# Performance work log

Measured on AMD Instinct MI355X. Metric: run time of the kernel, lower is better.

The kernel has to match this reference:

```python
import jax, jax.numpy as jnp
import numpy as np

NA, NT, E = 8000, 30000, 150000
H, C, HID = 4, 64, 64  # heads, per-head out_channels, hidden_dim
AF, TF = 32, 48


def _gat(x_src, x_dst, src, dst, W, a_src, a_dst, bias, n_dst):
    # PyG GATConv, concat=False, add_self_loops=False, eval (no dropout)
    h_src = (x_src @ W).reshape(-1, H, C)          # [Ns,H,C]
    h_dst = (x_dst @ W).reshape(-1, H, C)          # [Nd,H,C]
    al_s = jnp.sum(h_src * a_src, axis=-1)         # [Ns,H]
    al_d = jnp.sum(h_dst * a_dst, axis=-1)         # [Nd,H]
    e = jax.nn.leaky_relu(al_s[src] + al_d[dst], 0.2)  # [E,H]
    m = jax.ops.segment_max(e, dst, num_segments=n_dst)
    m = jnp.where(jnp.isfinite(m), m, 0.0)
    ex = jnp.exp(e - m[dst])
    den = jax.ops.segment_sum(ex, dst, num_segments=n_dst)
    alpha = ex / (den[dst] + 1e-16)                # per-dst softmax
    out = jax.ops.segment_sum(alpha[:, :, None] * h_src[src], dst, num_segments=n_dst)
    return jnp.mean(out, axis=1) + bias            # mean over heads + bias


def _bn(x, g, b):  # BatchNorm1d, training-mode batch stats, biased var
    mu = jnp.mean(x, axis=0)
    v = jnp.var(x, axis=0)
    return g * (x - mu) * jax.lax.rsqrt(v + 1e-5) + b


def _ln(x, g, b):
    mu = jnp.mean(x, axis=-1, keepdims=True)
    v = jnp.var(x, axis=-1, keepdims=True)
    return g * (x - mu) * jax.lax.rsqrt(v + 1e-5) + b


def setup_inputs() -> dict:
    key = jax.random.key(0)
    ks = jax.random.split(key, 40)
    n = lambda i, shp, s=0.05: jax.random.normal(ks[i], shp, jnp.float32) * s
    ri = lambda i, hi: jax.random.randint(ks[i], (E,), 0, hi, jnp.int32)
    inp = {
        'x_agent': jax.random.normal(ks[0], (NA, AF), jnp.float32),
        'x_track': jax.random.normal(ks[1], (NT, TF), jnp.float32),
        'ei_a2t1_src': ri(2, NA), 'ei_a2t1_dst': ri(3, NT),
        'ei_t2a1_src': ri(4, NT), 'ei_t2a1_dst': ri(5, NA),
        'ei_a2t2_src': ri(6, NA), 'ei_a2t2_dst': ri(7, NT),
        'ei_t2a2_src': ri(8, NT), 'ei_t2a2_dst': ri(9, NA),
        'ae_W': n(10, (AF, HID)), 'ae_b': jnp.zeros((HID,), jnp.float32),
        'te_W': n(11, (TF, HID)), 'te_b': jnp.zeros((HID,), jnp.float32),
        # stacked GATConv params: [layer=3, relation=4, ...]; rel order: a2t1,t2a1,a2t2,t2a2
        'conv_W': n(12, (3, 4, HID, H * C)),
        'conv_asrc': n(13, (3, 4, H, C)),
        'conv_adst': n(14, (3, 4, H, C)),
        'conv_bias': jnp.zeros((3, 4, C), jnp.float32),
        'bn_gamma': jnp.ones((3, 2, HID), jnp.float32),   # [layer, agent/track, HID]
        'bn_beta': jnp.zeros((3, 2, HID), jnp.float32),
        # actor heads: 0=agent_alpha,1=agent_beta,2=track_alpha,3=track_beta
        'actor_W1': n(15, (4, HID, HID // 2)), 'actor_b1': jnp.zeros((4, HID // 2), jnp.float32),
        'actor_g': jnp.ones((4, HID // 2), jnp.float32), 'actor_be': jnp.zeros((4, HID // 2), jnp.float32),
        'actor_W2': n(16, (4, HID // 2, 1)), 'actor_b2': jnp.zeros((4, 1), jnp.float32),
        # critic global value head
        'cW1': n(17, (HID * 6, HID * 2)), 'cb1': jnp.zeros((HID * 2,), jnp.float32),
        'cg1': jnp.ones((HID * 2,), jnp.float32), 'cbe1': jnp.zeros((HID * 2,), jnp.float32),
        'cW2': n(18, (HID * 2, HID)), 'cb2': jnp.zeros((HID,), jnp.float32),
        'cg2': jnp.ones((HID,), jnp.float32), 'cbe2': jnp.zeros((HID,), jnp.float32),
        'cW3': n(19, (HID, HID // 2)), 'cb3': jnp.zeros((HID // 2,), jnp.float32),
        'cW4': n(20, (HID // 2, 1)), 'cb4': jnp.zeros((1,), jnp.float32),
    }
    return inp


def _forward(x_agent, x_track,
             ei_a2t1_src, ei_a2t1_dst, ei_t2a1_src, ei_t2a1_dst,
             ei_a2t2_src, ei_a2t2_dst, ei_t2a2_src, ei_t2a2_dst,
             ae_W, ae_b, te_W, te_b,
             conv_W, conv_asrc, conv_adst, conv_bias,
             bn_gamma, bn_beta,
             actor_W1, actor_b1, actor_g, actor_be, actor_W2, actor_b2,
             cW1, cb1, cg1, cbe1, cW2, cb2, cg2, cbe2, cW3, cb3, cW4, cb4):
    xa = jax.nn.relu(x_agent @ ae_W + ae_b)
    xt = jax.nn.relu(x_track @ te_W + te_b)
    prev_a, prev_t = None, None
    for l in range(3):
        # HeteroConv aggr='mean': track <- mean(rel0, rel2); agent <- mean(rel1, rel3)
        ot = 0.5 * (_gat(xa, xt, ei_a2t1_src, ei_a2t1_dst, conv_W[l, 0], conv_asrc[l, 0], conv_adst[l, 0], conv_bias[l, 0], NT)
                    + _gat(xa, xt, ei_a2t2_src, ei_a2t2_dst, conv_W[l, 2], conv_asrc[l, 2], conv_adst[l, 2], conv_bias[l, 2], NT))
        oa = 0.5 * (_gat(xt, xa, ei_t2a1_src, ei_t2a1_dst, conv_W[l, 1], conv_asrc[l, 1], conv_adst[l, 1], conv_bias[l, 1], NA)
                    + _gat(xt, xa, ei_t2a2_src, ei_t2a2_dst, conv_W[l, 3], conv_asrc[l, 3], conv_adst[l, 3], conv_bias[l, 3], NA))
        oa = _bn(jax.nn.relu(oa), bn_gamma[l, 0], bn_beta[l, 0])
        ot = _bn(jax.nn.relu(ot), bn_gamma[l, 1], bn_beta[l, 1])
        if l > 0:  # residuals after layers 2 and 3
            oa = oa + prev_a
            ot = ot + prev_t
        prev_a, prev_t = oa, ot
        xa, xt = oa, ot

    def head(x, i):
        h = jax.nn.relu(_ln(x @ actor_W1[i] + actor_b1[i], actor_g[i], actor_be[i]))
        return jax.nn.softplus(h @ actor_W2[i] + actor_b2[i]) + 1.0

    aA, aB = head(xa, 0), head(xa, 1)
    tA, tB = head(xt, 2), head(xt, 3)
    aC = aA / (aA + aB)
    tC = tA / (tA + tB)

    # critic global value (torch.std is unbiased, ddof=1)
    g = jnp.concatenate([
        jnp.mean(xa, axis=0), jnp.max(xa, axis=0), jnp.std(xa, axis=0, ddof=1),
        jnp.mean(xt, axis=0), jnp.max(xt, axis=0), jnp.std(xt, axis=0, ddof=1)], axis=0)[None, :]
    h = jax.nn.relu(_ln(g @ cW1 + cb1, cg1, cbe1))
    h = jax.nn.relu(_ln(h @ cW2 + cb2, cg2, cbe2))
    h = jax.nn.relu(h @ cW3 + cb3)
    gv = jnp.squeeze(h @ cW4 + cb4)
    return aA, aB, aC, tA, tB, tC, gv


def reference(x_agent, x_track,
              ei_a2t1_src, ei_a2t1_dst, ei_t2a1_src, ei_t2a1_dst,
              ei_a2t2_src, ei_a2t2_dst, ei_t2a2_src, ei_t2a2_dst,
              ae_W, ae_b, te_W, te_b,
              conv_W, conv_asrc, conv_adst, conv_bias,
              bn_gamma, bn_beta,
              actor_W1, actor_b1, actor_g, actor_be, actor_W2, actor_b2,
              cW1, cb1, cg1, cbe1, cW2, cb2, cg2, cbe2, cW3, cb3, cW4, cb4):
    return _forward(x_agent, x_track,
                    ei_a2t1_src, ei_a2t1_dst, ei_t2a1_src, ei_t2a1_dst,
                    ei_a2t2_src, ei_a2t2_dst, ei_t2a2_src, ei_t2a2_dst,
                    ae_W, ae_b, te_W, te_b,
                    conv_W, conv_asrc, conv_adst, conv_bias,
                    bn_gamma, bn_beta,
                    actor_W1, actor_b1, actor_g, actor_be, actor_W2, actor_b2,
                    cW1, cb1, cg1, cbe1, cW2, cb2, cg2, cbe2, cW3, cb3, cW4, cb4)
```

## Files before the change

### kernel.cpp

```cpp
#include <hip/hip_runtime.h>
#include <math.h>

#define NAg 8000
#define NTr 30000
#define NE  150000

#define XA_OFF 0
#define XT_OFF 512000
#define H0_OFF 2432000
#define H1_OFF 4480000
#define H2_OFF 12160000
#define H3_OFF 14208000
#define BNSTB 8320000
#define WVB   8336384
#define W2B   8342528
#define ALS0 21888000
#define ALS1 21920000
#define ALS2 22040000
#define ALS3 22072000
#define ALD0 22192000
#define ALD1 22312000
#define ALD2 22344000
#define ALD3 22464000
#define ESRC_I 22496000
#define OAACC 23104000
#define OTACC 23616000
#define BNST 25536000
#define CST  25536256
#define ROWP_I 25536640
#define CURS_I 25656704
#define RELSTRIDE 30016

typedef unsigned short ushortT;

__device__ __forceinline__ float lrelu(float x){ return x >= 0.f ? x : 0.2f*x; }
__device__ __forceinline__ unsigned fmap(float f){ unsigned u=__float_as_uint(f); return (u&0x80000000u)? ~u : (u|0x80000000u); }
__device__ __forceinline__ float funmap(unsigned u){ return (u&0x80000000u)? __uint_as_float(u&0x7FFFFFFFu) : __uint_as_float(~u); }
__device__ __forceinline__ float softplusf(float x){ return fmaxf(x,0.f) + log1pf(expf(-fabsf(x))); }
__device__ __forceinline__ ushortT f2bf(float f){
  unsigned u = __float_as_uint(f);
  unsigned r = u + 0x7FFFu + ((u>>16)&1u);
  return (ushortT)(r>>16);
}
__device__ __forceinline__ float bf2f(ushortT s){ return __uint_as_float(((unsigned)s)<<16); }
__device__ __forceinline__ float wred64(float v){
  #pragma unroll
  for (int o=32;o;o>>=1) v += __shfl_xor(v,o);
  return v;
}
__device__ __forceinline__ float wred32(float v){
  #pragma unroll
  for (int o=16;o;o>>=1) v += __shfl_xor(v,o,32);
  return v;
}
__device__ __forceinline__ int selH(int r){ return r==0?H0_OFF: r==1?H1_OFF: r==2?H2_OFF:H3_OFF; }
__device__ __forceinline__ int selALS(int r){ return r==0?ALS0: r==1?ALS1: r==2?ALS2:ALS3; }
__device__ __forceinline__ int selALD(int r){ return r==0?ALD0: r==1?ALD1: r==2?ALD2:ALD3; }

__device__ __forceinline__ float agg_rel(const int* es, int p, int p1, const float* als,
                                         const ushortT* h16, float ad, int lane, int hh, int base) {
  float num0=0.f, num1=0.f, num2=0.f, num3=0.f, den=0.f;
  for (; p + 4 <= p1; p += 4) {
    int sa = es[p], sb = es[p+1], sc = es[p+2], sd4 = es[p+3];
    ushort4 va = *(const ushort4*)(h16 + (size_t)sa*256 + lane*4);
    ushort4 vb = *(const ushort4*)(h16 + (size_t)sb*256 + lane*4);
    ushort4 vc = *(const ushort4*)(h16 + (size_t)sc*256 + lane*4);
    ushort4 vd = *(const ushort4*)(h16 + (size_t)sd4*256 + lane*4);
    float la = als[sa*4+hh], lb = als[sb*4+hh], lc = als[sc*4+hh], ld = als[sd4*4+hh];
    float ea = __expf(lrelu(la + ad));
    float eb = __expf(lrelu(lb + ad));
    float ec = __expf(lrelu(lc + ad));
    float ed = __expf(lrelu(ld + ad));
    den += (ea+eb)+(ec+ed);
    float qa0=__shfl(ea,base), qa1=__shfl(ea,base+1), qa2=__shfl(ea,base+2), qa3=__shfl(ea,base+3);
    float qb0=__shfl(eb,base), qb1=__shfl(eb,base+1), qb2=__shfl(eb,base+2), qb3=__shfl(eb,base+3);
    float qc0=__shfl(ec,base), qc1=__shfl(ec,base+1), qc2=__shfl(ec,base+2), qc3=__shfl(ec,base+3);
    float qd0=__shfl(ed,base), qd1=__shfl(ed,base+1), qd2=__shfl(ed,base+2), qd3=__shfl(ed,base+3);
    num0 += qa0*bf2f(va.x) + qb0*bf2f(vb.x) + qc0*bf2f(vc.x) + qd0*bf2f(vd.x);
    num1 += qa1*bf2f(va.y) + qb1*bf2f(vb.y) + qc1*bf2f(vc.y) + qd1*bf2f(vd.y);
    num2 += qa2*bf2f(va.z) + qb2*bf2f(vb.z) + qc2*bf2f(vc.z) + qd2*bf2f(vd.z);
    num3 += qa3*bf2f(va.w) + qb3*bf2f(vb.w) + qc3*bf2f(vc.w) + qd3*bf2f(vd.w);
  }
  for (; p < p1; ++p) {
    int s = es[p];
    ushort4 va = *(const ushort4*)(h16 + (size_t)s*256 + lane*4);
    float e = __expf(lrelu(als[s*4 + hh] + ad));
    den += e;
    float q0 = __shfl(e, base), q1 = __shfl(e, base+1), q2 = __shfl(e, base+2), q3 = __shfl(e, base+3);
    num0 += q0*bf2f(va.x); num1 += q1*bf2f(va.y); num2 += q2*bf2f(va.z); num3 += q3*bf2f(va.w);
  }
  float rd = 1.f/(den + 1e-16f);
  float r0 = __shfl(rd, base), r1 = __shfl(rd, base+1), r2 = __shfl(rd, base+2), r3 = __shfl(rd, base+3);
  return num0*r0 + num1*r1 + num2*r2 + num3*r3;
}

__global__ __launch_bounds__(256) void k_encoder(const float* xA, const float* xT,
    const float* aeW, const float* aeB, const float* teW, const float* teB, float* ws) {
  int bid = blockIdx.x;
  int t = threadIdx.x, wv = t >> 6, lane = t & 63;
  if (bid < 2 && t < 192) ws[CST + bid*192 + t] = 0.f;
  int type, nb;
  if (bid < 2000) { type = 0; nb = bid; } else { type = 1; nb = bid - 2000; }
  int N = type ? NTr : NAg;
  int n = nb*4 + wv;
  int F = type ? 48 : 32;
  const float* X = type ? xT : xA;
  const float* W = type ? teW : aeW;
  const float* B = type ? teB : aeB;
  float* out = ws + (type ? XT_OFF : XA_OFF);
  __shared__ float xs[4][48];
  if (n < N && lane < F) xs[wv][lane] = X[(size_t)n*F + lane];
  __syncthreads();
  if (n >= N) return;
  float acc = B[lane];
  for (int k = 0; k < F; ++k) acc += xs[wv][k] * W[k*64 + lane];
  out[(size_t)n*64 + lane] = fmaxf(acc, 0.f);
}

__global__ __launch_bounds__(256) void k_hist(const int* d0_,const int* d1_,const int* d2_,const int* d3_,
                                              int* wsi) {
  int r = blockIdx.y;
  const int* dp = r==0? d0_ : r==1? d1_ : r==2? d2_ : d3_;
  int e = blockIdx.x*256 + threadIdx.x;
  if (e >= NE) return;
  atomicAdd(&wsi[ROWP_I + r*RELSTRIDE + dp[e]], 1);
}

__global__ __launch_bounds__(256) void k_scan(int* wsi) {
  int r = blockIdx.x;
  int n = ((r & 1) ? NAg : NTr) + 1;
  int* rp = wsi + ROWP_I + r*RELSTRIDE;
  __shared__ int part[256];
  int t = threadIdx.x;
  int chunk = (n + 255) / 256;
  int lo = t*chunk, hi = min(lo + chunk, n);
  int s = 0;
  for (int i = lo; i < hi; ++i) s += rp[i];
  part[t] = s;
  __syncthreads();
  if (t == 0) {
    int run = 0;
    for (int i = 0; i < 256; ++i) { int tm = part[i]; part[i] = run; run += tm; }
  }
  __syncthreads();
  int run = part[t];
  for (int i = lo; i < hi; ++i) { int tm = rp[i]; rp[i] = run; run += tm; }
}

__global__ __launch_bounds__(256) void k_fill(const int* s0,const int* d0_,const int* s1,const int* d1_,
    const int* s2,const int* d2_,const int* s3,const int* d3_, int* wsi) {
  int r = blockIdx.y;
  const int* sp = r==0? s0 : r==1? s1 : r==2? s2 : s3;
  const int* dp = r==0? d0_ : r==1? d1_ : r==2? d2_ : d3_;
  int e = blockIdx.x*256 + threadIdx.x;
  if (e >= NE) return;
  int d = dp[e];
  int pos = wsi[ROWP_I + r*RELSTRIDE + d] + atomicAdd(&wsi[CURS_I + r*RELSTRIDE + d], 1);
  wsi[ESRC_I + r*NE + pos] = sp[e];
}

__global__ __launch_bounds__(256) void k_wprep2(const float* convW, const float* convAsrc,
                                                const float* convAdst, float* ws) {
  int lr = blockIdx.x;
  int layer = lr >> 2, r = lr & 3;
  const float* W = convW + (size_t)lr*64*256;
  float* W2 = ws + W2B + (size_t)lr*64*256;
  int t = threadIdx.x;
  int c = t >> 2, h = t & 3;
  for (int k = 0; k < 64; ++k) W2[k*256 + t] = W[k*256 + h*64 + c];
  int k = t >> 2;
  const float* ad = convAdst + (size_t)lr*256;
  const float* as = convAsrc + (size_t)lr*256;
  float s0 = 0.f, s1 = 0.f;
  for (int cc = 0; cc < 64; ++cc) {
    float w = W[k*256 + h*64 + cc];
    s0 += w * ad[h*64 + cc];
    s1 += w * as[h*64 + cc];
  }
  ws[WVB + (size_t)(layer*8 + 0*4 + r)*256 + t] = s0;
  ws[WVB + (size_t)(layer*8 + 1*4 + r)*256 + t] = s1;
}

__global__ __launch_bounds__(256) void k_alx(float* ws, int layer) {
  int bid = blockIdx.x;
  int t = threadIdx.x;
  if (bid < 64) ws[BNSTB + bid*256 + t] = 0.f;
  int y, b0;
  if (bid < 7500)       { y = 0; b0 = bid; }
  else if (bid < 9500)  { y = 1; b0 = bid - 7500; }
  else if (bid < 17000) { y = 2; b0 = bid - 9500; }
  else if (bid < 19000) { y = 3; b0 = bid - 17000; }
  else if (bid < 21000) { y = 4; b0 = bid - 19000; }
  else if (bid < 28500) { y = 5; b0 = bid - 21000; }
  else if (bid < 30500) { y = 6; b0 = bid - 28500; }
  else                  { y = 7; b0 = bid - 30500; }
  int side = y >> 2, r = y & 3;
  int wv = t >> 6, lane = t & 63;
  int n = b0*4 + wv;
  const float* xv = ws + (side ? ((r & 1) ? XT_OFF : XA_OFF) : ((r & 1) ? XA_OFF : XT_OFF));
  float4 wv4 = *(const float4*)(ws + WVB + (size_t)(layer*8 + y)*256 + lane*4);
  float xk = xv[(size_t)n*64 + lane];
  float p0 = wred64(xk * wv4.x);
  float p1 = wred64(xk * wv4.y);
  float p2 = wred64(xk * wv4.z);
  float p3 = wred64(xk * wv4.w);
  if (lane == 0) {
    float4 o; o.x = p0; o.y = p1; o.z = p2; o.w = p3;
    *(float4*)(ws + (side ? selALS(r) : selALD(r)) + (size_t)n*4) = o;
  }
}

__global__ __launch_bounds__(256) void k_hgemm(float* ws, int layer) {
  int tile = blockIdx.x;
  int r, row0;
  if (tile < 500)        { r = 0; row0 = tile*16; }
  else if (tile < 2375)  { r = 1; row0 = (tile-500)*16; }
  else if (tile < 2875)  { r = 2; row0 = (tile-2375)*16; }
  else                   { r = 3; row0 = (tile-2875)*16; }
  const float* W2 = ws + W2B + (size_t)(layer*4 + r)*64*256;
  const float* xg = ws + ((r & 1) ? XT_OFF : XA_OFF);
  ushortT* h16 = (ushortT*)(ws + selH(r));
  __shared__ float xs[16][64];
  int t = threadIdx.x;
  #pragma unroll
  for (int i = 0; i < 4; ++i) {
    int lin = i*256 + t;
    xs[lin>>6][lin&63] = xg[((size_t)row0 + (lin>>6))*64 + (lin&63)];
  }
  __syncthreads();
  int c0 = t & 63;
  int tr = t >> 6;
  float acc[4][4];
  #pragma unroll
  for (int i=0;i<4;i++){ acc[i][0]=0;acc[i][1]=0;acc[i][2]=0;acc[i][3]=0; }
  const float* Wc = W2 + c0*4;
  for (int k4 = 0; k4 < 16; ++k4) {
    float4 xv[4];
    #pragma unroll
    for (int i = 0; i < 4; ++i) xv[i] = *(const float4*)&xs[tr*4+i][k4*4];
    #pragma unroll
    for (int kk = 0; kk < 4; ++kk) {
      int k = k4*4 + kk;
      float4 w4 = *(const float4*)(Wc + k*256);
      #pragma unroll
      for (int i = 0; i < 4; ++i) {
        float x = (kk==0)?xv[i].x:(kk==1)?xv[i].y:(kk==2)?xv[i].z:xv[i].w;
        acc[i][0] += x*w4.x; acc[i][1] += x*w4.y; acc[i][2] += x*w4.z; acc[i][3] += x*w4.w;
      }
    }
  }
  #pragma unroll
  for (int i = 0; i < 4; ++i) {
    int row = row0 + tr*4 + i;
    ushort4 pk;
    pk.x = f2bf(acc[i][0]); pk.y = f2bf(acc[i][1]);
    pk.z = f2bf(acc[i][2]); pk.w = f2bf(acc[i][3]);
    *(ushort4*)(h16 + (size_t)row*256 + c0*4) = pk;
  }
}

__global__ __launch_bounds__(256) void k_agg(const float* convBias, float* ws, int layer) {
  int t = threadIdx.x, wv = t >> 6, lane = t & 63, hh = lane & 3, base = lane & ~3;
  const int* wsi = (const int*)ws;
  int bid = blockIdx.x;
  __shared__ float part[4][64];
  __shared__ float sh1[4][64];
  __shared__ float sh2[4][64];
  if (bid < 4000) {
    int node = bid*2 + (wv >> 1);
    int rr = wv & 1;
    int r = rr ? 3 : 1;
    const int* rp = wsi + ROWP_I + r*RELSTRIDE;
    const int* es = wsi + ESRC_I + r*NE;
    const float* als = ws + selALS(r);
    const ushortT* h16 = (const ushortT*)(ws + selH(r));
    float ad = (ws + selALD(r))[node*4 + hh];
    part[wv][lane] = agg_rel(es, rp[node], rp[node+1], als, h16, ad, lane, hh, base);
    __syncthreads();
    if (rr == 0) {
      float o = part[wv][lane] + part[wv+1][lane];
      float bavg = 0.5f*(convBias[(layer*4 + 1)*64 + lane] + convBias[(layer*4 + 3)*64 + lane]);
      float z = fmaxf(o*0.125f + bavg, 0.f);
      ws[OAACC + (size_t)node*64 + lane] = z;
      sh1[wv][lane] = z; sh2[wv][lane] = z*z;
    } else {
      sh1[wv][lane] = 0.f; sh2[wv][lane] = 0.f;
    }
    __syncthreads();
    if (t < 64) {
      float s1 = sh1[0][t] + sh1[1][t] + sh1[2][t] + sh1[3][t];
      float s2 = sh2[0][t] + sh2[1][t] + sh2[2][t] + sh2[3][t];
      int bucket = bid & 63;
      atomicAdd(&ws[BNSTB + bucket*256 + t], s1);
      atomicAdd(&ws[BNSTB + bucket*256 + 64 + t], s2);
    }
  } else {
    int node = (bid - 4000)*4 + wv;
    float outv = 0.f;
    #pragma unroll
    for (int rr = 0; rr < 2; ++rr) {
      int r = rr ? 2 : 0;
      const int* rp = wsi + ROWP_I + r*RELSTRIDE;
      const int* es = wsi + ESRC_I + r*NE;
      const float* als = ws + selALS(r);
      const ushortT* h16 = (const ushortT*)(ws + selH(r));
      float ad = (ws + selALD(r))[node*4 + hh];
      outv += agg_rel(es, rp[node], rp[node+1], als, h16, ad, lane, hh, base);
    }
    float bavg = 0.5f*(convBias[(layer*4 + 0)*64 + lane] + convBias[(layer*4 + 2)*64 + lane]);
    float z = fmaxf(outv*0.125f + bavg, 0.f);
    ws[OTACC + (size_t)node*64 + lane] = z;
    sh1[wv][lane] = z; sh2[wv][lane] = z*z;
    __syncthreads();
    if (t < 64) {
      float s1 = sh1[0][t] + sh1[1][t] + sh1[2][t] + sh1[3][t];
      float s2 = sh2[0][t] + sh2[1][t] + sh2[2][t] + sh2[3][t];
      int bucket = bid & 63;
      atomicAdd(&ws[BNSTB + bucket*256 + 128 + t], s1);
      atomicAdd(&ws[BNSTB + bucket*256 + 192 + t], s2);
    }
  }
}

__global__ __launch_bounds__(256) void k_bnred(float* ws) {
  int t = threadIdx.x;
  float s = 0.f;
  #pragma unroll
  for (int b = 0; b < 64; ++b) s += ws[BNSTB + b*256 + t];
  ws[BNST + t] = s;
}

__global__ __launch_bounds__(256) void k_bnnorm(const float* bnG, const float* bnB, float* ws, int layer) {
  int bid = blockIdx.x;
  int type, i;
  if (bid < 2000) { type = 0; i = bid*256 + threadIdx.x; }
  else            { type = 1; i = (bid - 2000)*256 + threadIdx.x; }
  float* acc = ws + (type ? OTACC : OAACC);
  float* x = ws + (type ? XT_OFF : XA_OFF);
  int c = i & 63;
  float Nf = type ? 30000.f : 8000.f;
  float s1 = ws[BNST + type*128 + c], s2 = ws[BNST + type*128 + 64 + c];
  float mu = s1/Nf, var = s2/Nf - mu*mu;
  float g = bnG[(layer*2 + type)*64 + c], b = bnB[(layer*2 + type)*64 + c];
  float y = g*(acc[i]-mu)*rsqrtf(var + 1e-5f) + b;
  if (layer > 0) y += x[i];
  x[i] = y;
}

__global__ __launch_bounds__(256) void k_actor(const float* aW1, const float* ab1, const float* ag,
    const float* abe, const float* aW2, const float* ab2, const float* ws, float* out) {
  int bid = blockIdx.x;
  int type, nb;
  if (bid < 2000) { type = 0; nb = bid; } else { type = 1; nb = bid - 2000; }
  int t = threadIdx.x, wv = t >> 6, lane = t & 63;
  int p = lane >> 5, j = lane & 31;
  int n = nb*4 + wv;
  const float* xg = ws + (type ? XT_OFF : XA_OFF);
  __shared__ float xsh[4][64];
  xsh[wv][lane] = xg[(size_t)n*64 + lane];
  __syncthreads();
  int i = (type ? 2 : 0) + p;
  const float* W = aW1 + i*2048 + j;
  float a0 = 0.f, a1 = 0.f, a2 = 0.f, a3 = 0.f;
  #pragma unroll
  for (int k = 0; k < 64; k += 4) {
    a0 += xsh[wv][k]   * W[k*32];
    a1 += xsh[wv][k+1] * W[(k+1)*32];
    a2 += xsh[wv][k+2] * W[(k+2)*32];
    a3 += xsh[wv][k+3] * W[(k+3)*32];
  }
  float tv = ((a0+a1)+(a2+a3)) + ab1[i*32 + j];
  float mu = wred32(tv) * (1.f/32.f);
  float dz = tv - mu;
  float var = wred32(dz*dz) * (1.f/32.f);
  float hn = fmaxf(ag[i*32+j]*dz*rsqrtf(var + 1e-5f) + abe[i*32+j], 0.f);
  float s = wred32(hn * aW2[i*32 + j]) + ab2[i];
  float val = softplusf(s) + 1.f;
  float vA = __shfl(val, 0);
  float vB = __shfl(val, 32);
  if (lane == 0) {
    int offA = type ? 24000 : 0, offB = type ? 54000 : 8000, offC = type ? 84000 : 16000;
    out[offA + n] = vA;
    out[offB + n] = vB;
    out[offC + n] = vA / (vA + vB);
  }
}

__global__ __launch_bounds__(256) void k_criticstats(float* ws) {
  int type = blockIdx.y;
  int N = type ? NTr : NAg;
  const float* x = ws + (type ? XT_OFF : XA_OFF);
  int t = threadIdx.x;
  int c = t & 63;
  float s1 = 0.f, s2 = 0.f, mx = -3.4e38f;
  for (int n = blockIdx.x*4 + (t>>6); n < N; n += gridDim.x*4) {
    float v = x[(size_t)n*64 + c];
    s1 += v; s2 += v*v; mx = fmaxf(mx, v);
  }
  __shared__ float sd[3][256];
  sd[0][t]=s1; sd[1][t]=s2; sd[2][t]=mx;
  __syncthreads();
  if (t < 64) {
    s1 = sd[0][t]+sd[0][t+64]+sd[0][t+128]+sd[0][t+192];
    s2 = sd[1][t]+sd[1][t+64]+sd[1][t+128]+sd[1][t+192];
    mx = fmaxf(fmaxf(sd[2][t],sd[2][t+64]), fmaxf(sd[2][t+128],sd[2][t+192]));
    atomicAdd(&ws[CST + type*192 + c], s1);
    atomicAdd(&ws[CST + type*192 + 64 + c], s2);
    atomicMax((unsigned*)&ws[CST + type*192 + 128 + c], fmap(mx));
  }
}

__device__ __forceinline__ float blocksum128(float v, float* red) {
  int t = threadIdx.x;
  red[t] = v; __syncthreads();
  #pragma unroll
  for (int s = 64; s > 0; s >>= 1) { if (t < s) red[t] += red[t+s]; __syncthreads(); }
  float r = red[0]; __syncthreads();
  return r;
}

__global__ __launch_bounds__(128) void k_critic(const float* cW1,const float* cb1,const float* cg1,const float* cbe1,
    const float* cW2,const float* cb2,const float* cg2,const float* cbe2,
    const float* cW3,const float* cb3,const float* cW4,const float* cb4,
    const float* ws, float* out) {
  __shared__ float g[384];
  __shared__ float h1[128];
  __shared__ float h2s[64];
  __shared__ float red[128];
  int t = threadIdx.x;
  if (t < 64) {
    #pragma unroll
    for (int type = 0; type < 2; ++type) {
      float Nf = type ? 30000.f : 8000.f;
      float s1 = ws[CST + type*192 + t];
      float s2 = ws[CST + type*192 + 64 + t];
      unsigned mu_ = __float_as_uint(ws[CST + type*192 + 128 + t]);
      float mean = s1 / Nf;
      float sd = sqrtf(fmaxf((s2 - Nf*mean*mean) / (Nf - 1.f), 0.f));
      g[type*192 + t] = mean;
      g[type*192 + 64 + t] = funmap(mu_);
      g[type*192 + 128 + t] = sd;
    }
  }
  __syncthreads();
  float v = cb1[t];
  for (int k = 0; k < 384; ++k) v += g[k] * cW1[k*128 + t];
  float mu = blocksum128(v, red) * (1.f/128.f);
  float d = v - mu;
  float var = blocksum128(d*d, red) * (1.f/128.f);
  h1[t] = fmaxf(cg1[t]*d*rsqrtf(var + 1e-5f) + cbe1[t], 0.f);
  __syncthreads();
  float v2 = 0.f;
  if (t < 64) { v2 = cb2[t]; for (int k = 0; k < 128; ++k) v2 += h1[k] * cW2[k*64 + t]; }
  float mu2 = blocksum128(t < 64 ? v2 : 0.f, red) * (1.f/64.f);
  float d2 = v2 - mu2;
  float var2 = blocksum128(t < 64 ? d2*d2 : 0.f, red) * (1.f/64.f);
  if (t < 64) h2s[t] = fmaxf(cg2[t]*d2*rsqrtf(var2 + 1e-5f) + cbe2[t], 0.f);
  __syncthreads();
  float v3 = 0.f;
  if (t < 32) {
    v3 = cb3[t];
    for (int k = 0; k < 64; ++k) v3 += h2s[k] * cW3[k*32 + t];
    v3 = fmaxf(v3, 0.f);
  }
  float s4 = blocksum128(t < 32 ? v3 * cW4[t] : 0.f, red);
  if (t == 0) out[114000] = s4 + cb4[0];
}

extern "C" void kernel_launch(void* const* d_in, const int* in_sizes, int n_in,
                              void* d_out, int out_size, void* d_ws, size_t ws_size,
                              hipStream_t stream) {
  const float* x_agent = (const float*)d_in[0];
  const float* x_track = (const float*)d_in[1];
  const int* s0 = (const int*)d_in[2]; const int* d0_ = (const int*)d_in[3];
  const int* s1 = (const int*)d_in[4]; const int* d1_ = (const int*)d_in[5];
  const int* s2 = (const int*)d_in[6]; const int* d2_ = (const int*)d_in[7];
  const int* s3 = (const int*)d_in[8]; const int* d3_ = (const int*)d_in[9];
  const float* aeW = (const float*)d_in[10]; const float* aeB = (const float*)d_in[11];
  const float* teW = (const float*)d_in[12]; const float* teB = (const float*)d_in[13];
  const float* convW    = (const float*)d_in[14];
  const float* convAsrc = (const float*)d_in[15];
  const float* convAdst = (const float*)d_in[16];
  const float* convBias = (const float*)d_in[17];
  const float* bnG = (const float*)d_in[18]; const float* bnB = (const float*)d_in[19];
  const float* aW1 = (const float*)d_in[20]; const float* ab1 = (const float*)d_in[21];
  const float* ag  = (const float*)d_in[22]; const float* abe = (const float*)d_in[23];
  const float* aW2 = (const float*)d_in[24]; const float* ab2 = (const float*)d_in[25];
  const float* cW1 = (const float*)d_in[26]; const float* cb1 = (const float*)d_in[27];
  const float* cg1 = (const float*)d_in[28]; const float* cbe1 = (const float*)d_in[29];
  const float* cW2 = (const float*)d_in[30]; const float* cb2 = (const float*)d_in[31];
  const float* cg2 = (const float*)d_in[32]; const float* cbe2 = (const float*)d_in[33];
  const float* cW3 = (const float*)d_in[34]; const float* cb3 = (const float*)d_in[35];
  const float* cW4 = (const float*)d_in[36]; const float* cb4 = (const float*)d_in[37];
  float* ws = (float*)d_ws;
  int* wsi = (int*)d_ws;
  float* out = (float*)d_out;

  hipMemsetAsync(wsi + ROWP_I, 0, (size_t)240128 * sizeof(int), stream);

  k_encoder<<<dim3(9500), 256, 0, stream>>>(x_agent, x_track, aeW, aeB, teW, teB, ws);

  k_hist<<<dim3(586, 4), 256, 0, stream>>>(d0_, d1_, d2_, d3_, wsi);
  k_scan<<<dim3(4), 256, 0, stream>>>(wsi);
  k_fill<<<dim3(586, 4), 256, 0, stream>>>(s0,d0_,s1,d1_,s2,d2_,s3,d3_, wsi);
  k_wprep2<<<dim3(12), 256, 0, stream>>>(convW, convAsrc, convAdst, ws);

  for (int l = 0; l < 3; ++l) {
    k_alx<<<dim3(38000), 256, 0, stream>>>(ws, l);
    k_hgemm<<<dim3(4750), 256, 0, stream>>>(ws, l);
    k_agg<<<dim3(11500), 256, 0, stream>>>(convBias, ws, l);
    k_bnred<<<1, 256, 0, stream>>>(ws);
    k_bnnorm<<<dim3(9500), 256, 0, stream>>>(bnG, bnB, ws, l);
  }

  k_criticstats<<<dim3(128, 2), 256, 0, stream>>>(ws);
  k_actor<<<dim3(9500), 256, 0, stream>>>(aW1, ab1, ag, abe, aW2, ab2, ws, out);
  k_critic<<<1, 128, 0, stream>>>(cW1,cb1,cg1,cbe1,cW2,cb2,cg2,cbe2,cW3,cb3,cW4,cb4, ws, out);
}
```

Measured before the change: 659.0 us.

## Merge preprocessing kernels and fuse critic stats into final batchnorm

Merges the encoder, edge histogram and weight-prep kernels into one launch that dispatches on block index. It also fuses the last layer's batchnorm with the critic's sum, sum-of-squares and max statistics, writing them into 64 bucketed partial arrays that the critic kernel then reduces. This removes several kernel launches and one full re-read of the node features. In exchange it adds a bucketed scratch buffer that must be zeroed each run, and a 64-way reduction loop inside the single-block critic.

```diff
diff --git a/kernel.cpp b/kernel.cpp
--- a/kernel.cpp
+++ b/kernel.cpp
@@ -14,6 +14,7 @@
 #define BNSTB 8320000
 #define WVB   8336384
 #define W2B   8342528
+#define CSTB  18100000
 #define ALS0 21888000
 #define ALS1 21920000
 #define ALS2 22040000
@@ -26,7 +27,6 @@
 #define OAACC 23104000
 #define OTACC 23616000
 #define BNST 25536000
-#define CST  25536256
 #define ROWP_I 25536640
 #define CURS_I 25656704
 #define RELSTRIDE 30016
@@ -94,36 +94,53 @@
   return num0*r0 + num1*r1 + num2*r2 + num3*r3;
 }
 
-__global__ __launch_bounds__(256) void k_encoder(const float* xA, const float* xT,
-    const float* aeW, const float* aeB, const float* teW, const float* teB, float* ws) {
+__global__ __launch_bounds__(256) void k_pre(const float* xA, const float* xT,
+    const float* aeW, const float* aeB, const float* teW, const float* teB,
+    const int* d0_, const int* d1_, const int* d2_, const int* d3_,
+    const float* convW, const float* convAsrc, const float* convAdst, float* ws) {
   int bid = blockIdx.x;
-  int t = threadIdx.x, wv = t >> 6, lane = t & 63;
-  if (bid < 2 && t < 192) ws[CST + bid*192 + t] = 0.f;
-  int type, nb;
-  if (bid < 2000) { type = 0; nb = bid; } else { type = 1; nb = bid - 2000; }
-  int N = type ? NTr : NAg;
-  int n = nb*4 + wv;
-  int F = type ? 48 : 32;
-  const float* X = type ? xT : xA;
-  const float* W = type ? teW : aeW;
-  const float* B = type ? teB : aeB;
-  float* out = ws + (type ? XT_OFF : XA_OFF);
+  int t = threadIdx.x;
   __shared__ float xs[4][48];
-  if (n < N && lane < F) xs[wv][lane] = X[(size_t)n*F + lane];
-  __syncthreads();
-  if (n >= N) return;
-  float acc = B[lane];
-  for (int k = 0; k < F; ++k) acc += xs[wv][k] * W[k*64 + lane];
-  out[(size_t)n*64 + lane] = fmaxf(acc, 0.f);
-}
-
-__global__ __launch_bounds__(256) void k_hist(const int* d0_,const int* d1_,const int* d2_,const int* d3_,
-                                              int* wsi) {
-  int r = blockIdx.y;
-  const int* dp = r==0? d0_ : r==1? d1_ : r==2? d2_ : d3_;
-  int e = blockIdx.x*256 + threadIdx.x;
-  if (e >= NE) return;
-  atomicAdd(&wsi[ROWP_I + r*RELSTRIDE + dp[e]], 1);
+  if (bid < 9500) {
+    int wv = t >> 6, lane = t & 63;
+    int type, nb;
+    if (bid < 2000) { type = 0; nb = bid; } else { type = 1; nb = bid - 2000; }
+    int n = nb*4 + wv;
+    int F = type ? 48 : 32;
+    const float* X = type ? xT : xA;
+    const float* W = type ? teW : aeW;
+    const float* B = type ? teB : aeB;
+    float* out = ws + (type ? XT_OFF : XA_OFF);
+    if (lane < F) xs[wv][lane] = X[(size_t)n*F + lane];
+    __syncthreads();
+    float acc = B[lane];
+    for (int k = 0; k < F; ++k) acc += xs[wv][k] * W[k*64 + lane];
+    out[(size_t)n*64 + lane] = fmaxf(acc, 0.f);
+  } else if (bid < 11844) {
+    int idx = bid - 9500;
+    int r = idx / 586, eb = idx % 586;
+    const int* dp = r==0? d0_ : r==1? d1_ : r==2? d2_ : d3_;
+    int e = eb*256 + t;
+    if (e < NE) atomicAdd(&((int*)ws)[ROWP_I + r*RELSTRIDE + dp[e]], 1);
+  } else {
+    int lr = bid - 11844;
+    int layer = lr >> 2, r = lr & 3;
+    const float* W = convW + (size_t)lr*64*256;
+    float* W2 = ws + W2B + (size_t)lr*64*256;
+    int c = t >> 2, h = t & 3;
+    for (int k = 0; k < 64; ++k) W2[k*256 + t] = W[k*256 + h*64 + c];
+    int k = t >> 2;
+    const float* ad = convAdst + (size_t)lr*256;
+    const float* as = convAsrc + (size_t)lr*256;
+    float s0 = 0.f, s1 = 0.f;
+    for (int cc = 0; cc < 64; ++cc) {
+      float w = W[k*256 + h*64 + cc];
+      s0 += w * ad[h*64 + cc];
+      s1 += w * as[h*64 + cc];
+    }
+    ws[WVB + (size_t)(layer*8 + 0*4 + r)*256 + t] = s0;
+    ws[WVB + (size_t)(layer*8 + 1*4 + r)*256 + t] = s1;
+  }
 }
 
 __global__ __launch_bounds__(256) void k_scan(int* wsi) {
@@ -157,28 +174,6 @@
   int d = dp[e];
   int pos = wsi[ROWP_I + r*RELSTRIDE + d] + atomicAdd(&wsi[CURS_I + r*RELSTRIDE + d], 1);
   wsi[ESRC_I + r*NE + pos] = sp[e];
-}
-
-__global__ __launch_bounds__(256) void k_wprep2(const float* convW, const float* convAsrc,
-                                                const float* convAdst, float* ws) {
-  int lr = blockIdx.x;
-  int layer = lr >> 2, r = lr & 3;
-  const float* W = convW + (size_t)lr*64*256;
-  float* W2 = ws + W2B + (size_t)lr*64*256;
-  int t = threadIdx.x;
-  int c = t >> 2, h = t & 3;
-  for (int k = 0; k < 64; ++k) W2[k*256 + t] = W[k*256 + h*64 + c];
-  int k = t >> 2;
-  const float* ad = convAdst + (size_t)lr*256;
-  const float* as = convAsrc + (size_t)lr*256;
-  float s0 = 0.f, s1 = 0.f;
-  for (int cc = 0; cc < 64; ++cc) {
-    float w = W[k*256 + h*64 + cc];
-    s0 += w * ad[h*64 + cc];
-    s1 += w * as[h*64 + cc];
-  }
-  ws[WVB + (size_t)(layer*8 + 0*4 + r)*256 + t] = s0;
-  ws[WVB + (size_t)(layer*8 + 1*4 + r)*256 + t] = s1;
 }
 
 __global__ __launch_bounds__(256) void k_alx(float* ws, int layer) {
@@ -322,12 +317,15 @@
   }
 }
 
-__global__ __launch_bounds__(256) void k_bnred(float* ws) {
+__global__ __launch_bounds__(256) void k_bnred2(float* ws, int zero_cstb) {
   int t = threadIdx.x;
   float s = 0.f;
   #pragma unroll
   for (int b = 0; b < 64; ++b) s += ws[BNSTB + b*256 + t];
   ws[BNST + t] = s;
+  if (zero_cstb) {
+    for (int i = t; i < 24576; i += 256) ws[CSTB + i] = 0.f;
+  }
 }
 
 __global__ __launch_bounds__(256) void k_bnnorm(const float* bnG, const float* bnB, float* ws, int layer) {
@@ -347,6 +345,36 @@
   x[i] = y;
 }
 
+__global__ __launch_bounds__(256) void k_bncrit(const float* bnG, const float* bnB, float* ws) {
+  int bid = blockIdx.x;
+  int t = threadIdx.x;
+  int type, i0;
+  if (bid < 2000) { type = 0; i0 = bid*256; }
+  else            { type = 1; i0 = (bid-2000)*256; }
+  float* acc = ws + (type ? OTACC : OAACC);
+  float* x = ws + (type ? XT_OFF : XA_OFF);
+  int i = i0 + t;
+  int c = i & 63;
+  float Nf = type ? 30000.f : 8000.f;
+  float s1 = ws[BNST + type*128 + c], s2 = ws[BNST + type*128 + 64 + c];
+  float mu = s1/Nf, var = s2/Nf - mu*mu;
+  float g = bnG[(2*2+type)*64 + c], b = bnB[(2*2+type)*64 + c];
+  float y = g*(acc[i]-mu)*rsqrtf(var+1e-5f) + b + x[i];
+  x[i] = y;
+  __shared__ float sd[3][256];
+  sd[0][t] = y; sd[1][t] = y*y; sd[2][t] = y;
+  __syncthreads();
+  if (t < 64) {
+    float a1 = sd[0][t]+sd[0][t+64]+sd[0][t+128]+sd[0][t+192];
+    float a2 = sd[1][t]+sd[1][t+64]+sd[1][t+128]+sd[1][t+192];
+    float mx = fmaxf(fmaxf(sd[2][t],sd[2][t+64]), fmaxf(sd[2][t+128],sd[2][t+192]));
+    int bucket = bid & 63;
+    atomicAdd(&ws[CSTB + bucket*384 + type*192 + t], a1);
+    atomicAdd(&ws[CSTB + bucket*384 + type*192 + 64 + t], a2);
+    atomicMax((unsigned*)&ws[CSTB + bucket*384 + type*192 + 128 + t], fmap(mx));
+  }
+}
+
 __global__ __launch_bounds__(256) void k_actor(const float* aW1, const float* ab1, const float* ag,
     const float* abe, const float* aW2, const float* ab2, const float* ws, float* out) {
   int bid = blockIdx.x;
@@ -386,30 +414,6 @@
   }
 }
 
-__global__ __launch_bounds__(256) void k_criticstats(float* ws) {
-  int type = blockIdx.y;
-  int N = type ? NTr : NAg;
-  const float* x = ws + (type ? XT_OFF : XA_OFF);
-  int t = threadIdx.x;
-  int c = t & 63;
-  float s1 = 0.f, s2 = 0.f, mx = -3.4e38f;
-  for (int n = blockIdx.x*4 + (t>>6); n < N; n += gridDim.x*4) {
-    float v = x[(size_t)n*64 + c];
-    s1 += v; s2 += v*v; mx = fmaxf(mx, v);
-  }
-  __shared__ float sd[3][256];
-  sd[0][t]=s1; sd[1][t]=s2; sd[2][t]=mx;
-  __syncthreads();
-  if (t < 64) {
-    s1 = sd[0][t]+sd[0][t+64]+sd[0][t+128]+sd[0][t+192];
-    s2 = sd[1][t]+sd[1][t+64]+sd[1][t+128]+sd[1][t+192];
-    mx = fmaxf(fmaxf(sd[2][t],sd[2][t+64]), fmaxf(sd[2][t+128],sd[2][t+192]));
-    atomicAdd(&ws[CST + type*192 + c], s1);
-    atomicAdd(&ws[CST + type*192 + 64 + c], s2);
-    atomicMax((unsigned*)&ws[CST + type*192 + 128 + c], fmap(mx));
-  }
-}
-
 __device__ __forceinline__ float blocksum128(float v, float* red) {
   int t = threadIdx.x;
   red[t] = v; __syncthreads();
@@ -431,10 +435,15 @@
   if (t < 64) {
     #pragma unroll
     for (int type = 0; type < 2; ++type) {
+      float s1 = 0.f, s2 = 0.f;
+      unsigned mu_ = 0u;
+      for (int b2 = 0; b2 < 64; ++b2) {
+        s1 += ws[CSTB + b2*384 + type*192 + t];
+        s2 += ws[CSTB + b2*384 + type*192 + 64 + t];
+        unsigned u = __float_as_uint(ws[CSTB + b2*384 + type*192 + 128 + t]);
+        mu_ = max(mu_, u);
+      }
       float Nf = type ? 30000.f : 8000.f;
-      float s1 = ws[CST + type*192 + t];
-      float s2 = ws[CST + type*192 + 64 + t];
-      unsigned mu_ = __float_as_uint(ws[CST + type*192 + 128 + t]);
       float mean = s1 / Nf;
       float sd = sqrtf(fmaxf((s2 - Nf*mean*mean) / (Nf - 1.f), 0.f));
       g[type*192 + t] = mean;
@@ -498,22 +507,20 @@
 
   hipMemsetAsync(wsi + ROWP_I, 0, (size_t)240128 * sizeof(int), stream);
 
-  k_encoder<<<dim3(9500), 256, 0, stream>>>(x_agent, x_track, aeW, aeB, teW, teB, ws);
-
-  k_hist<<<dim3(586, 4), 256, 0, stream>>>(d0_, d1_, d2_, d3_, wsi);
+  k_pre<<<dim3(11856), 256, 0, stream>>>(x_agent, x_track, aeW, aeB, teW, teB,
+                                         d0_, d1_, d2_, d3_, convW, convAsrc, convAdst, ws);
   k_scan<<<dim3(4), 256, 0, stream>>>(wsi);
   k_fill<<<dim3(586, 4), 256, 0, stream>>>(s0,d0_,s1,d1_,s2,d2_,s3,d3_, wsi);
-  k_wprep2<<<dim3(12), 256, 0, stream>>>(convW, convAsrc, convAdst, ws);
 
   for (int l = 0; l < 3; ++l) {
     k_alx<<<dim3(38000), 256, 0, stream>>>(ws, l);
     k_hgemm<<<dim3(4750), 256, 0, stream>>>(ws, l);
     k_agg<<<dim3(11500), 256, 0, stream>>>(convBias, ws, l);
-    k_bnred<<<1, 256, 0, stream>>>(ws);
-    k_bnnorm<<<dim3(9500), 256, 0, stream>>>(bnG, bnB, ws, l);
-  }
-
-  k_criticstats<<<dim3(128, 2), 256, 0, stream>>>(ws);
+    k_bnred2<<<dim3(1), 256, 0, stream>>>(ws, l == 2 ? 1 : 0);
+    if (l < 2) k_bnnorm<<<dim3(9500), 256, 0, stream>>>(bnG, bnB, ws, l);
+  }
+
+  k_bncrit<<<dim3(9500), 256, 0, stream>>>(bnG, bnB, ws);
   k_actor<<<dim3(9500), 256, 0, stream>>>(aW1, ab1, ag, abe, aW2, ab2, ws, out);
   k_critic<<<1, 128, 0, stream>>>(cW1,cb1,cg1,cbe1,cW2,cb2,cg2,cbe2,cW3,cb3,cW4,cb4, ws, out);
 }
```

Result: no change. 653.0 us (-0.9%).
